# Kernel tuning notes

Measured on AMD Instinct MI355X. Metric: run time of the kernel, lower is better.

Reference implementation:

```python
import jax, jax.numpy as jnp
import numpy as np
import math

B, C, H, W = 2, 512, 64, 64
NUM_HEADS = 8
D_K = C // NUM_HEADS
SCALE = 1.0 / math.sqrt(D_K)


def setup_inputs() -> dict:
    key = jax.random.key(0)
    ks = jax.random.split(key, 7)
    init = 0.02
    return {
        "x": jax.random.normal(ks[0], (B, C, H, W), dtype=jnp.float32),
        "Wq": jax.random.normal(ks[1], (C, C), dtype=jnp.float32) * init,
        "bq": jnp.zeros((C,), dtype=jnp.float32),
        "Wkv": jax.random.normal(ks[2], (2 * C, C), dtype=jnp.float32) * init,
        "bkv": jnp.zeros((2 * C,), dtype=jnp.float32),
        "Wp": jax.random.normal(ks[3], (C, C), dtype=jnp.float32) * init,
        "bp": jnp.zeros((C,), dtype=jnp.float32),
    }


def _conv1x1(x, w, b):
    # x: [b, c_in, h, w], w: [c_out, c_in] (1x1 conv kernel), b: [c_out]
    return jnp.einsum('bchw,oc->bohw', x, w) + b[None, :, None, None]


def reference(x, Wq, bq, Wkv, bkv, Wp, bp):
    b, c, h, w = x.shape
    l = h * w
    q = _conv1x1(x, Wq, bq)
    kv = _conv1x1(x, Wkv, bkv)
    k, v = jnp.split(kv, 2, axis=1)
    # reshape to [b, heads, d_k, l]
    q = q.reshape(b, NUM_HEADS, D_K, l)
    k = k.reshape(b, NUM_HEADS, D_K, l)
    v = v.reshape(b, NUM_HEADS, D_K, l)
    attn = jnp.einsum('bhct,bhcs->bhts', q, k) * SCALE  # [b,h,l,l]
    attn = jax.nn.softmax(attn, axis=-1)
    out = jnp.einsum('bhts,bhcs->bhct', attn, v)  # [b,h,d_k,l]
    out = out.reshape(b, c, h, w)
    out = _conv1x1(out, Wp, bp)
    return out
```

## Files before the change

kernel.cpp:

```cpp
#include <hip/hip_runtime.h>
#include <math.h>

#define L_SEQ 4096
#define C_DIM 512
#define NH 8
#define DK 64
#define NB 2
#define QSC 0.18033688011112042f

typedef _Float16 f16;
typedef _Float16 f16x8 __attribute__((ext_vector_type(8)));
typedef _Float16 f16x4 __attribute__((ext_vector_type(4)));
typedef __fp16 h16x2 __attribute__((ext_vector_type(2)));
typedef float f32x4 __attribute__((ext_vector_type(4)));
typedef float f32x16 __attribute__((ext_vector_type(16)));
typedef unsigned int u32;

__global__ __launch_bounds__(256) void prep(
    const float* __restrict__ X, const float* __restrict__ Wq,
    const float* __restrict__ Wkv, const float* __restrict__ Wp,
    f16* __restrict__ Xt, f16* __restrict__ Wqkh,
    f16* __restrict__ Wvh, f16* __restrict__ Wph)
{
    const int tid = threadIdx.x;
    const int z = blockIdx.z;
    if (z < 2) {
        __shared__ f16 Ts[64][72];
        const float* src = X + (size_t)z * C_DIM * L_SEQ;
        f16* dst = Xt + (size_t)z * L_SEQ * C_DIM;
        for (int tile = blockIdx.x; tile < 512; tile += gridDim.x) {
            const int c0 = (tile & 7) * 64;
            const int t0 = (tile >> 3) * 64;
            __syncthreads();
            #pragma unroll
            for (int p = 0; p < 4; ++p) {
                const int c = (tid >> 4) + p * 16;
                const int t = (tid & 15) * 4;
                const float4 v = *(const float4*)(src + (size_t)(c0 + c) * L_SEQ + t0 + t);
                Ts[t + 0][c] = (f16)v.x; Ts[t + 1][c] = (f16)v.y;
                Ts[t + 2][c] = (f16)v.z; Ts[t + 3][c] = (f16)v.w;
            }
            __syncthreads();
            #pragma unroll
            for (int p = 0; p < 2; ++p) {
                const int t = (tid >> 3) + p * 32;
                const int ch = (tid & 7) * 8;
                *(f16x8*)(dst + (size_t)(t0 + t) * C_DIM + c0 + ch) =
                    *(const f16x8*)&Ts[t][ch];
            }
        }
    } else {
        const float* srcs[4] = {Wq, Wkv, Wkv + 262144, Wp};
        f16* dsts[4] = {Wqkh, Wqkh + 262144, Wvh, Wph};
        #pragma unroll
        for (int s = 0; s < 4; ++s) {
            const float* sp = srcs[s]; f16* dp = dsts[s];
            for (int i = blockIdx.x * 256 + tid; i < 65536; i += gridDim.x * 256) {
                const float4 v = *(const float4*)(sp + (size_t)i * 4);
                f16x4 h; h[0] = (f16)v.x; h[1] = (f16)v.y; h[2] = (f16)v.z; h[3] = (f16)v.w;
                *(f16x4*)(dp + (size_t)i * 4) = h;
            }
        }
    }
}

__global__ __launch_bounds__(256) void qkv_mfma(
    const f16* __restrict__ Xt, const f16* __restrict__ Wqkv,
    const float* __restrict__ bq, const float* __restrict__ bkv,
    f16* __restrict__ Qh, f16* __restrict__ Kh, f16* __restrict__ Vh)
{
    __shared__ f16 As[128][40];
    __shared__ f16 Bs[128][40];
    const int tid = threadIdx.x;
    const int lane = tid & 63, w = tid >> 6;
    const int l15 = lane & 15, quad = lane >> 4;
    const int wy = w >> 1, wx = w & 1;
    const int mb0 = blockIdx.x * 128;
    const int n0  = blockIdx.y * 128;

    f32x4 acc[4][4] = {};
    const int row = tid >> 2, c8 = (tid & 3) * 8;
    const f16* aptr = Xt + (size_t)mb0 * 512;
    const f16* bptr = Wqkv + (size_t)n0 * 512;

    uint4 ga0 = *(const uint4*)(aptr + (size_t)row * 512 + c8);
    uint4 ga1 = *(const uint4*)(aptr + (size_t)(row + 64) * 512 + c8);
    uint4 gb0 = *(const uint4*)(bptr + (size_t)row * 512 + c8);
    uint4 gb1 = *(const uint4*)(bptr + (size_t)(row + 64) * 512 + c8);

    for (int k0 = 0; k0 < 512; k0 += 32) {
        __syncthreads();
        *(uint4*)&As[row][c8] = ga0;
        *(uint4*)&As[row + 64][c8] = ga1;
        *(uint4*)&Bs[row][c8] = gb0;
        *(uint4*)&Bs[row + 64][c8] = gb1;
        if (k0 + 32 < 512) {
            ga0 = *(const uint4*)(aptr + (size_t)row * 512 + k0 + 32 + c8);
            ga1 = *(const uint4*)(aptr + (size_t)(row + 64) * 512 + k0 + 32 + c8);
            gb0 = *(const uint4*)(bptr + (size_t)row * 512 + k0 + 32 + c8);
            gb1 = *(const uint4*)(bptr + (size_t)(row + 64) * 512 + k0 + 32 + c8);
        }
        __syncthreads();
        f16x8 af[4], bf[4];
        #pragma unroll
        for (int i = 0; i < 4; ++i)
            af[i] = *(const f16x8*)&As[wy * 64 + i * 16 + l15][quad * 8];
        #pragma unroll
        for (int n = 0; n < 4; ++n)
            bf[n] = *(const f16x8*)&Bs[wx * 64 + n * 16 + l15][quad * 8];
        #pragma unroll
        for (int i = 0; i < 4; ++i)
            #pragma unroll
            for (int n = 0; n < 4; ++n)
                acc[i][n] = __builtin_amdgcn_mfma_f32_16x16x32_f16(af[i], bf[n], acc[i][n], 0, 0, 0);
    }

    const int qp = ((quad & 1) << 1) | (quad >> 1);

    #pragma unroll
    for (int nn = 0; nn < 4; ++nn) {
        const int o = n0 + wx * 64 + nn * 16 + l15;
        if (o < 1024) {
            const bool isQ = (o < 512);
            const float bias = isQ ? bq[o] : bkv[o - 512];
            const int h = (o & 511) >> 6, d = o & 63;
            f16* base = isQ ? Qh : Kh;
            #pragma unroll
            for (int i = 0; i < 4; ++i) {
                const int tr = mb0 + wy * 64 + i * 16 + quad * 4;
                #pragma unroll
                for (int r = 0; r < 4; ++r) {
                    const int tg = tr + r;
                    const int bh = (tg >> 12) * NH + h;
                    float v = acc[i][nn][r] + bias;
                    if (isQ) v *= QSC;
                    base[((size_t)bh * L_SEQ + (tg & 4095)) * DK + d] = (f16)v;
                }
            }
        } else {
            const int c = o - 1024;
            const float bias = bkv[512 + c];
            const int h = c >> 6, d = c & 63;
            #pragma unroll
            for (int i = 0; i < 4; ++i) {
                const int trp = mb0 + wy * 64 + i * 16 + qp * 4;
                #pragma unroll
                for (int r = 0; r < 4; ++r) {
                    const int tq = trp + r;
                    const int bh = (tq >> 12) * NH + h;
                    const float v = acc[i][nn][r] + bias;
                    Vh[((size_t)bh * DK + d) * L_SEQ + (tq & 4095)] = (f16)v;
                }
            }
        }
    }
}

__global__ __launch_bounds__(256) void oproj2(
    const f16* __restrict__ Bsrc, const f16* __restrict__ Wh,
    const float* __restrict__ bias, float* __restrict__ outP)
{
    __shared__ f16 As[64][40];
    __shared__ f16 Bs[128][40];
    const int tid = threadIdx.x;
    const int lane = tid & 63, w = tid >> 6;
    const int l15 = lane & 15, quad = lane >> 4;
    const int wy = w >> 1, wx = w & 1;
    const int n0  = blockIdx.x * 128;
    const int mb0 = blockIdx.y * 64;

    f32x4 acc[2][4] = {};
    const int row = tid >> 2, c8 = (tid & 3) * 8;
    const f16* aptr = Wh + (size_t)mb0 * 512;
    const f16* bptr = Bsrc + (size_t)n0 * 512;

    uint4 ga0 = *(const uint4*)(aptr + (size_t)row * 512 + c8);
    uint4 gb0 = *(const uint4*)(bptr + (size_t)row * 512 + c8);
    uint4 gb1 = *(const uint4*)(bptr + (size_t)(row + 64) * 512 + c8);

    for (int k0 = 0; k0 < 512; k0 += 32) {
        __syncthreads();
        *(uint4*)&As[row][c8] = ga0;
        *(uint4*)&Bs[row][c8] = gb0;
        *(uint4*)&Bs[row + 64][c8] = gb1;
        if (k0 + 32 < 512) {
            ga0 = *(const uint4*)(aptr + (size_t)row * 512 + k0 + 32 + c8);
            gb0 = *(const uint4*)(bptr + (size_t)row * 512 + k0 + 32 + c8);
            gb1 = *(const uint4*)(bptr + (size_t)(row + 64) * 512 + k0 + 32 + c8);
        }
        __syncthreads();
        f16x8 af[2], bf[4];
        #pragma unroll
        for (int i = 0; i < 2; ++i)
            af[i] = *(const f16x8*)&As[wy * 32 + i * 16 + l15][quad * 8];
        #pragma unroll
        for (int n = 0; n < 4; ++n)
            bf[n] = *(const f16x8*)&Bs[wx * 64 + n * 16 + l15][quad * 8];
        #pragma unroll
        for (int i = 0; i < 2; ++i)
            #pragma unroll
            for (int n = 0; n < 4; ++n)
                acc[i][n] = __builtin_amdgcn_mfma_f32_16x16x32_f16(af[i], bf[n], acc[i][n], 0, 0, 0);
    }

    #pragma unroll
    for (int i = 0; i < 2; ++i) {
        #pragma unroll
        for (int r = 0; r < 4; ++r) {
            const int o = mb0 + wy * 32 + i * 16 + quad * 4 + r;
            const float bv = bias[o];
            #pragma unroll
            for (int nn = 0; nn < 4; ++nn) {
                const int tg = n0 + wx * 64 + nn * 16 + l15;
                outP[((size_t)(tg >> 12) * C_DIM + o) * L_SEQ + (tg & 4095)] =
                    acc[i][nn][r] + bv;
            }
        }
    }
}

__device__ __forceinline__ void gload_lds16(const char* g, char* l) {
    __builtin_amdgcn_global_load_lds(
        (const __attribute__((address_space(1))) void*)g,
        (__attribute__((address_space(3))) void*)l, 16, 0, 0);
}

union FR { u32 u[4]; f16x8 v; };

__device__ __forceinline__ void pack8(const f32x16& S, FR* fr, int base) {
    #pragma unroll
    for (int q = 0; q < 4; ++q) {
        const h16x2 a01 = __builtin_amdgcn_cvt_pkrtz(
            __builtin_amdgcn_exp2f(S[4 * q + 0]),
            __builtin_amdgcn_exp2f(S[4 * q + 1]));
        const h16x2 a23 = __builtin_amdgcn_cvt_pkrtz(
            __builtin_amdgcn_exp2f(S[4 * q + 2]),
            __builtin_amdgcn_exp2f(S[4 * q + 3]));
        union { h16x2 h; u32 u; } p0, p1; p0.h = a01; p1.h = a23;
        fr[base + (q >> 1)].u[(q & 1) * 2 + 0] = p0.u;
        fr[base + (q >> 1)].u[(q & 1) * 2 + 1] = p1.u;
    }
}

__global__ __launch_bounds__(256, 2) void flash16(
    const f16* __restrict__ Qh, const f16* __restrict__ Kh,
    const f16* __restrict__ Vh, f16* __restrict__ Oh)
{
    __shared__ f16 KS[2][4096];
    __shared__ f16 VS[3][4096];
    const int tid = threadIdx.x;
    const int lane = tid & 63, w = tid >> 6;
    const int l31 = lane & 31, hl = lane >> 5;
    const int bh = blockIdx.x;
    const int t0 = blockIdx.y * 128;
    const int wtb = t0 + w * 32;
    const f16* Qg = Qh + (size_t)bh * L_SEQ * DK;
    const char* Kg = (const char*)(Kh + (size_t)bh * L_SEQ * DK);
    const char* Vg = (const char*)(Vh + (size_t)bh * DK * L_SEQ);

    f16x8 qf[4];
    #pragma unroll
    for (int kst = 0; kst < 4; ++kst)
        qf[kst] = *(const f16x8*)(Qg + (size_t)(wtb + l31) * DK + kst * 16 + hl * 8);

    const int c0 = tid, c1 = tid + 256;
    const int kofs0 = (c0 >> 3) * 128  + (((c0 & 7) * 16) ^ (((c0 >> 3) & 7) << 4));
    const int kofs1 = (c1 >> 3) * 128  + (((c1 & 7) * 16) ^ (((c1 >> 3) & 7) << 4));
    const int vofs0 = (c0 >> 3) * 8192 + (((c0 & 7) * 16) ^ (((c0 >> 3) & 7) << 4));
    const int vofs1 = (c1 >> 3) * 8192 + (((c1 & 7) * 16) ^ (((c1 >> 3) & 7) << 4));
    const int lb0 = (w * 64) * 16, lb1 = (256 + w * 64) * 16;

    #define STAGE_K(kb, s0v) do {                                    \
        const char* kg_ = Kg + (size_t)(s0v) * 128;                  \
        char* kl_ = (char*)&KS[kb][0];                               \
        gload_lds16(kg_ + kofs0, kl_ + lb0);                         \
        gload_lds16(kg_ + kofs1, kl_ + lb1);                         \
    } while (0)
    #define STAGE_V(vOfs, s0v) do {                                  \
        const char* vg_ = Vg + (size_t)(s0v) * 2;                    \
        char* vl_ = (char*)&VS[0][0] + (vOfs);                       \
        gload_lds16(vg_ + vofs0, vl_ + lb0);                         \
        gload_lds16(vg_ + vofs1, vl_ + lb1);                         \
    } while (0)

    f32x16 O0 = {}, O1 = {};
    f32x16 Lacc = {};
    f16x8 onesv;
    #pragma unroll
    for (int j = 0; j < 8; ++j) onesv[j] = (f16)1.f;
    FR frA[4], frB[4];

    STAGE_K(0, 0); STAGE_V(0, 0);
    __syncthreads();

    const int swz = (l31 & 7) << 4;
    const int rowA = l31 * 128, rowB = (32 + l31) * 128;

    #define QKBODY(s0v, kbR, kbS, DOSTG, DOPV, stO, pvO, frC, frP) do {     \
        if (DOSTG) { STAGE_K(kbS, (s0v) + 64); STAGE_V(stO, (s0v) + 64); }  \
        const char* Kb = (const char*)&KS[kbR][0];                          \
        f16x8 kf[4];                                                        \
        _Pragma("unroll")                                                   \
        for (int kst = 0; kst < 4; ++kst)                                   \
            kf[kst] = *(const f16x8*)(Kb + rowA + ((kst * 32 + hl * 16) ^ swz)); \
        {                                                                   \
            f32x16 Sa = {};                                                 \
            __builtin_amdgcn_s_setprio(1);                                  \
            _Pragma("unroll")                                               \
            for (int kst = 0; kst < 4; ++kst)                               \
                Sa = __builtin_amdgcn_mfma_f32_32x32x16_f16(kf[kst], qf[kst], Sa, 0, 0, 0); \
            __builtin_amdgcn_s_setprio(0);                                  \
            _Pragma("unroll")                                               \
            for (int kst = 0; kst < 4; ++kst)                               \
                kf[kst] = *(const f16x8*)(Kb + rowB + ((kst * 32 + hl * 16) ^ swz)); \
            pack8(Sa, frC, 0);                                              \
        }                                                                   \
        {                                                                   \
            f32x16 Sb = {};                                                 \
            __builtin_amdgcn_s_setprio(1);                                  \
            _Pragma("unroll")                                               \
            for (int kst = 0; kst < 4; ++kst)                               \
                Sb = __builtin_amdgcn_mfma_f32_32x32x16_f16(kf[kst], qf[kst], Sb, 0, 0, 0); \
            if (DOPV) {                                                     \
                const char* Vb = (const char*)&VS[0][0] + (pvO);            \
                _Pragma("unroll")                                           \
                for (int kst = 0; kst < 4; ++kst) {                         \
                    const int ca = (kst * 32 + hl * 16) ^ swz;              \
                    const f16x8 v0 = *(const f16x8*)(Vb + rowA + ca);       \
                    const f16x8 v1 = *(const f16x8*)(Vb + rowB + ca);       \
                    O0 = __builtin_amdgcn_mfma_f32_32x32x16_f16(v0, frP[kst].v, O0, 0, 0, 0); \
                    O1 = __builtin_amdgcn_mfma_f32_32x32x16_f16(v1, frP[kst].v, O1, 0, 0, 0); \
                }                                                           \
            }                                                               \
            __builtin_amdgcn_s_setprio(0);                                  \
            pack8(Sb, frC, 2);                                              \
            _Pragma("unroll")                                               \
            for (int kst = 0; kst < 4; ++kst)                               \
                Lacc = __builtin_amdgcn_mfma_f32_32x32x16_f16(onesv, frC[kst].v, Lacc, 0, 0, 0); \
        }                                                                   \
        __syncthreads();                                                    \
    } while (0)

    QKBODY(0, 0, 1, true, false, 8192, 0, frA, frB);

    int s0 = 64;
    int stO = 16384, pvO = 0;
    #pragma unroll 1
    for (int p = 0; p < 31; ++p) {
        QKBODY(s0, 1, 0, true, true, stO, pvO, frB, frA);
        s0 += 64; stO = (stO == 16384) ? 0 : stO + 8192; pvO = (pvO == 16384) ? 0 : pvO + 8192;
        QKBODY(s0, 0, 1, true, true, stO, pvO, frA, frB);
        s0 += 64; stO = (stO == 16384) ? 0 : stO + 8192; pvO = (pvO == 16384) ? 0 : pvO + 8192;
    }
    QKBODY(s0, 1, 0, false, true, 0, pvO, frB, frA);

    {
        const char* Vb = (const char*)&VS[0][0];
        __builtin_amdgcn_s_setprio(1);
        #pragma unroll
        for (int kst = 0; kst < 4; ++kst) {
            const int ca = (kst * 32 + hl * 16) ^ swz;
            const f16x8 v0 = *(const f16x8*)(Vb + rowA + ca);
            const f16x8 v1 = *(const f16x8*)(Vb + rowB + ca);
            O0 = __builtin_amdgcn_mfma_f32_32x32x16_f16(v0, frB[kst].v, O0, 0, 0, 0);
            O1 = __builtin_amdgcn_mfma_f32_32x32x16_f16(v1, frB[kst].v, O1, 0, 0, 0);
        }
        __builtin_amdgcn_s_setprio(0);
    }
    #undef QKBODY
    #undef STAGE_K
    #undef STAGE_V

    const float rinv = 1.f / Lacc[0];

    const int b = bh >> 3, h = bh & 7;
    f16* OhP = Oh + ((size_t)(b * L_SEQ + wtb + l31)) * C_DIM + h * DK;
    #pragma unroll
    for (int run = 0; run < 4; ++run) {
        f16x4 v0, v1;
        #pragma unroll
        for (int j = 0; j < 4; ++j) {
            v0[j] = (f16)(O0[run * 4 + j] * rinv);
            v1[j] = (f16)(O1[run * 4 + j] * rinv);
        }
        *(f16x4*)(OhP + run * 8 + 4 * hl) = v0;
        *(f16x4*)(OhP + 32 + run * 8 + 4 * hl) = v1;
    }
}

extern "C" void kernel_launch(void* const* d_in, const int* in_sizes, int n_in,
                              void* d_out, int out_size, void* d_ws, size_t ws_size,
                              hipStream_t stream) {
    (void)in_sizes; (void)n_in; (void)out_size; (void)ws_size;
    const float* x   = (const float*)d_in[0];
    const float* Wq  = (const float*)d_in[1];
    const float* bq  = (const float*)d_in[2];
    const float* Wkv = (const float*)d_in[3];
    const float* bkv = (const float*)d_in[4];
    const float* Wp  = (const float*)d_in[5];
    const float* bp  = (const float*)d_in[6];
    float* out = (float*)d_out;

    f16* Xt    = (f16*)d_ws;
    f16* Wqkh  = Xt + 4194304;
    f16* Wvh   = Wqkh + 524288;
    f16* Wph   = Wvh + 262144;
    f16* Qh    = Wph + 262144;
    f16* Kh    = Qh + 4194304;
    f16* Vh    = Kh + 4194304;
    f16* Oh    = Vh + 4194304;

    prep<<<dim3(128, 1, 3), 256, 0, stream>>>(x, Wq, Wkv, Wp, Xt, Wqkh, Wvh, Wph);
    qkv_mfma<<<dim3(64, 12), 256, 0, stream>>>(Xt, Wqkh, bq, bkv, Qh, Kh, Vh);
    flash16<<<dim3(16, 32), 256, 0, stream>>>(Qh, Kh, Vh, Oh);
    oproj2<<<dim3(64, 8), 256, 0, stream>>>(Oh, Wph, bp, out);
}
```

Measured before the change: 196.6 us.

## Load K tiles directly from global into registers, dropping K shared-memory staging

The K tile is no longer staged in shared memory. Each lane now loads its K fragments straight from global memory into double-buffered registers one tile ahead, and the LDS reads of K are gone. This removes LDS traffic and frees shared memory. In exchange it adds 32 more VGPRs of prefetch buffers, which may hurt occupancy under launch_bounds(256,2), and K rows are re-read by each of the 4 waves through the cache rather than loaded once per block.

New measurement: 241.3 us. 1.23x slower.

```diff
diff --git a/kernel.cpp b/kernel.cpp
--- a/kernel.cpp
+++ b/kernel.cpp
@@ -246,7 +246,6 @@
     const f16* __restrict__ Qh, const f16* __restrict__ Kh,
     const f16* __restrict__ Vh, f16* __restrict__ Oh)
 {
-    __shared__ f16 KS[2][4096];
     __shared__ f16 VS[3][4096];
     const int tid = threadIdx.x;
     const int lane = tid & 63, w = tid >> 6;
@@ -264,18 +263,10 @@
         qf[kst] = *(const f16x8*)(Qg + (size_t)(wtb + l31) * DK + kst * 16 + hl * 8);
 
     const int c0 = tid, c1 = tid + 256;
-    const int kofs0 = (c0 >> 3) * 128  + (((c0 & 7) * 16) ^ (((c0 >> 3) & 7) << 4));
-    const int kofs1 = (c1 >> 3) * 128  + (((c1 & 7) * 16) ^ (((c1 >> 3) & 7) << 4));
     const int vofs0 = (c0 >> 3) * 8192 + (((c0 & 7) * 16) ^ (((c0 >> 3) & 7) << 4));
     const int vofs1 = (c1 >> 3) * 8192 + (((c1 & 7) * 16) ^ (((c1 >> 3) & 7) << 4));
     const int lb0 = (w * 64) * 16, lb1 = (256 + w * 64) * 16;
 
-    #define STAGE_K(kb, s0v) do {                                    \
-        const char* kg_ = Kg + (size_t)(s0v) * 128;                  \
-        char* kl_ = (char*)&KS[kb][0];                               \
-        gload_lds16(kg_ + kofs0, kl_ + lb0);                         \
-        gload_lds16(kg_ + kofs1, kl_ + lb1);                         \
-    } while (0)
     #define STAGE_V(vOfs, s0v) do {                                  \
         const char* vg_ = Vg + (size_t)(s0v) * 2;                    \
         char* vl_ = (char*)&VS[0][0] + (vOfs);                       \
@@ -283,36 +274,44 @@
         gload_lds16(vg_ + vofs1, vl_ + lb1);                         \
     } while (0)
 
+    const char* KgL = Kg + (size_t)l31 * 128 + hl * 16;
+
     f32x16 O0 = {}, O1 = {};
     f32x16 Lacc = {};
     f16x8 onesv;
     #pragma unroll
     for (int j = 0; j < 8; ++j) onesv[j] = (f16)1.f;
     FR frA[4], frB[4];
-
-    STAGE_K(0, 0); STAGE_V(0, 0);
+    f16x8 k0a[4], k0b[4], k1a[4], k1b[4];
+
+    #pragma unroll
+    for (int kst = 0; kst < 4; ++kst) {
+        k0a[kst] = *(const f16x8*)(KgL + kst * 32);
+        k0b[kst] = *(const f16x8*)(KgL + 32 * 128 + kst * 32);
+    }
+    STAGE_V(0, 0);
     __syncthreads();
 
     const int swz = (l31 & 7) << 4;
     const int rowA = l31 * 128, rowB = (32 + l31) * 128;
 
-    #define QKBODY(s0v, kbR, kbS, DOSTG, DOPV, stO, pvO, frC, frP) do {     \
-        if (DOSTG) { STAGE_K(kbS, (s0v) + 64); STAGE_V(stO, (s0v) + 64); }  \
-        const char* Kb = (const char*)&KS[kbR][0];                          \
-        f16x8 kf[4];                                                        \
-        _Pragma("unroll")                                                   \
-        for (int kst = 0; kst < 4; ++kst)                                   \
-            kf[kst] = *(const f16x8*)(Kb + rowA + ((kst * 32 + hl * 16) ^ swz)); \
+    #define QKBODY(s0v, DOSTG, DOPV, stO, pvO, frC, frP, KCa, KCb, KNa, KNb) do { \
+        if (DOSTG) {                                                        \
+            const char* kg_ = KgL + (size_t)((s0v) + 64) * 128;             \
+            _Pragma("unroll")                                               \
+            for (int kst = 0; kst < 4; ++kst) {                             \
+                KNa[kst] = *(const f16x8*)(kg_ + kst * 32);                 \
+                KNb[kst] = *(const f16x8*)(kg_ + 32 * 128 + kst * 32);      \
+            }                                                               \
+            STAGE_V(stO, (s0v) + 64);                                       \
+        }                                                                   \
         {                                                                   \
             f32x16 Sa = {};                                                 \
             __builtin_amdgcn_s_setprio(1);                                  \
             _Pragma("unroll")                                               \
             for (int kst = 0; kst < 4; ++kst)                               \
-                Sa = __builtin_amdgcn_mfma_f32_32x32x16_f16(kf[kst], qf[kst], Sa, 0, 0, 0); \
+                Sa = __builtin_amdgcn_mfma_f32_32x32x16_f16(KCa[kst], qf[kst], Sa, 0, 0, 0); \
             __builtin_amdgcn_s_setprio(0);                                  \
-            _Pragma("unroll")                                               \
-            for (int kst = 0; kst < 4; ++kst)                               \
-                kf[kst] = *(const f16x8*)(Kb + rowB + ((kst * 32 + hl * 16) ^ swz)); \
             pack8(Sa, frC, 0);                                              \
         }                                                                   \
         {                                                                   \
@@ -320,7 +319,7 @@
             __builtin_amdgcn_s_setprio(1);                                  \
             _Pragma("unroll")                                               \
             for (int kst = 0; kst < 4; ++kst)                               \
-                Sb = __builtin_amdgcn_mfma_f32_32x32x16_f16(kf[kst], qf[kst], Sb, 0, 0, 0); \
+                Sb = __builtin_amdgcn_mfma_f32_32x32x16_f16(KCb[kst], qf[kst], Sb, 0, 0, 0); \
             if (DOPV) {                                                     \
                 const char* Vb = (const char*)&VS[0][0] + (pvO);            \
                 _Pragma("unroll")                                           \
@@ -341,18 +340,18 @@
         __syncthreads();                                                    \
     } while (0)
 
-    QKBODY(0, 0, 1, true, false, 8192, 0, frA, frB);
+    QKBODY(0, true, false, 8192, 0, frA, frB, k0a, k0b, k1a, k1b);
 
     int s0 = 64;
     int stO = 16384, pvO = 0;
     #pragma unroll 1
     for (int p = 0; p < 31; ++p) {
-        QKBODY(s0, 1, 0, true, true, stO, pvO, frB, frA);
+        QKBODY(s0, true, true, stO, pvO, frB, frA, k1a, k1b, k0a, k0b);
         s0 += 64; stO = (stO == 16384) ? 0 : stO + 8192; pvO = (pvO == 16384) ? 0 : pvO + 8192;
-        QKBODY(s0, 0, 1, true, true, stO, pvO, frA, frB);
+        QKBODY(s0, true, true, stO, pvO, frA, frB, k0a, k0b, k1a, k1b);
         s0 += 64; stO = (stO == 16384) ? 0 : stO + 8192; pvO = (pvO == 16384) ? 0 : pvO + 8192;
     }
-    QKBODY(s0, 1, 0, false, true, 0, pvO, frB, frA);
+    QKBODY(s0, false, true, 0, pvO, frB, frA, k1a, k1b, k0a, k0b);
 
     {
         const char* Vb = (const char*)&VS[0][0];
@@ -368,7 +367,6 @@
         __builtin_amdgcn_s_setprio(0);
     }
     #undef QKBODY
-    #undef STAGE_K
     #undef STAGE_V
 
     const float rinv = 1.f / Lacc[0];
```
